# Optimization experiments

Measured on AMD Instinct MI355X. Metric: run time of the kernel, lower is better.

Reference implementation:

```python
import jax, jax.numpy as jnp
import numpy as np

N = 8192
D = 1024
TIME_DECAY = 86400.0
EPS = 1e-10


def setup_inputs() -> dict:
    key = jax.random.key(0)
    ks = jax.random.split(key, 8)
    x = jax.random.normal(ks[0], (N, D), dtype=jnp.float32)
    # timestamps spanning ~10 days so decay bias is non-trivial
    timestamps = jax.random.uniform(ks[1], (N,), dtype=jnp.float32) * (10.0 * TIME_DECAY)
    s = 1.0 / np.sqrt(D)
    Wq = jax.random.normal(ks[2], (D, D), dtype=jnp.float32) * s
    bq = jnp.zeros((D,), dtype=jnp.float32)
    Wk = jax.random.normal(ks[3], (D, D), dtype=jnp.float32) * s
    bk = jnp.zeros((D,), dtype=jnp.float32)
    Wv = jax.random.normal(ks[4], (D, D), dtype=jnp.float32) * s
    bv = jnp.zeros((D,), dtype=jnp.float32)
    return {"x": x, "timestamps": timestamps, "Wq": Wq, "bq": bq,
            "Wk": Wk, "bk": bk, "Wv": Wv, "bv": bv}


def reference(x, timestamps, Wq, bq, Wk, bk, Wv, bv):
    scale = jnp.asarray(D ** 0.5, x.dtype)
    # torch nn.Linear: y = x @ W.T + b
    Q = x @ Wq.T + bq          # [N, D]
    K = x @ Wk.T + bk          # [N, D]
    V = x @ Wv.T + bv          # [N, D]
    time_diff = timestamps[:, None] - timestamps[None, :]   # [N, N]
    time_decay = jnp.exp(-jnp.abs(time_diff) / TIME_DECAY)  # [N, N]
    scores = (Q @ K.T) / scale + jnp.log(time_decay + EPS)  # [N, N]
    attn = jax.nn.softmax(scores, axis=-1)
    return attn @ V
```

## Files before the change

### kernel.cpp

```cpp
#include <hip/hip_runtime.h>


using half8   = __attribute__((ext_vector_type(8))) _Float16;
using half4   = __attribute__((ext_vector_type(4))) _Float16;
using floatx4 = __attribute__((ext_vector_type(4))) float;

__device__ __forceinline__ void gload_lds16(const void* g, void* l) {
  __builtin_amdgcn_global_load_lds((const __attribute__((address_space(1))) void*)g,
                                   (__attribute__((address_space(3))) void*)l,
                                   16, 0, 0);
}

template<int N> __device__ __forceinline__ void waitv() {
  if constexpr (N == 8)      asm volatile("s_waitcnt vmcnt(8)" ::: "memory");
  else if constexpr (N == 6) asm volatile("s_waitcnt vmcnt(6)" ::: "memory");
  else                       asm volatile("s_waitcnt vmcnt(0)" ::: "memory");
}

#define MFMA16(ar, br, accrow)                                              \
  _Pragma("unroll")                                                         \
  for (int i_ = 0; i_ < 4; ++i_)                                            \
    _Pragma("unroll")                                                       \
    for (int j_ = 0; j_ < 4; ++j_)                                          \
      accrow[i_][j_] = __builtin_amdgcn_mfma_f32_16x16x32_f16(              \
          ar[i_], br[j_], accrow[i_][j_], 0, 0, 0);

__device__ __forceinline__ void kloop_s(
    const _Float16* __restrict__ A, const _Float16* __restrict__ B,
    long rowBase, long colBase, int lda, int ldb, int K,
    _Float16* __restrict__ As, _Float16* __restrict__ Bs,
    floatx4 (&acc)[8][4])
{
  const int tid = threadIdx.x;
  const int w = tid >> 6, lane = tid & 63;
  const int q = lane >> 4, l15 = lane & 15;
  const int wr = w >> 2, wcn = w & 3;

  const int sc = ((lane & 7) ^ (lane >> 3)) << 3;
  const _Float16* Agp[4]; const _Float16* Bgp[4];
#pragma unroll
  for (int p = 0; p < 4; ++p) {
    Agp[p] = A + (rowBase + p * 64 + (tid >> 3)) * (long)lda + sc;
    Bgp[p] = B + (colBase + p * 64 + (tid >> 3)) * (long)ldb + sc;
  }
  const int ldsOff = tid * 8;

  const int aRow = wr * 128 + l15;
  const int bRow = wcn * 64 + l15;
  const int cx = l15 & 7;
  const int pc0 = (q ^ cx) << 3, pc1 = ((4 + q) ^ cx) << 3;

  auto stageA = [&](int t) {
    _Float16* dst = As + (t & 1) * 16384;
    const int ko = t << 6;
#pragma unroll
    for (int p = 0; p < 4; ++p) gload_lds16(Agp[p] + ko, dst + p * 4096 + ldsOff);
  };
  auto stageB = [&](int t) {
    _Float16* dst = Bs + (t & 1) * 16384;
    const int ko = t << 6;
#pragma unroll
    for (int p = 0; p < 4; ++p) gload_lds16(Bgp[p] + ko, dst + p * 4096 + ldsOff);
  };

  const int NT = K >> 6;
  stageA(0); stageB(0); stageA(1); stageB(1);
  waitv<8>(); __builtin_amdgcn_s_barrier();

  for (int t = 0; t < NT; ++t) {
    const _Float16* Asl = As + (t & 1) * 16384;
    const _Float16* Bsl = Bs + (t & 1) * 16384;
    half8 b0[4], b1[4], a0lo[4], a0hi[4], a1lo[4], a1hi[4];

#pragma unroll
    for (int j = 0; j < 4; ++j) b0[j]   = *(const half8*)&Bsl[(bRow + 16 * j) * 64 + pc0];
#pragma unroll
    for (int i = 0; i < 4; ++i) a0lo[i] = *(const half8*)&Asl[(aRow + 16 * i) * 64 + pc0];
#pragma unroll
    for (int i = 0; i < 4; ++i) a0hi[i] = *(const half8*)&Asl[(aRow + 16 * (4 + i)) * 64 + pc0];
    {
      floatx4 (&alo)[4][4] = *(floatx4(*)[4][4])&acc[0];
      MFMA16(a0lo, b0, alo);
    }
#pragma unroll
    for (int j = 0; j < 4; ++j) b1[j]   = *(const half8*)&Bsl[(bRow + 16 * j) * 64 + pc1];
#pragma unroll
    for (int i = 0; i < 4; ++i) a1lo[i] = *(const half8*)&Asl[(aRow + 16 * i) * 64 + pc1];
    {
      floatx4 (&ahi)[4][4] = *(floatx4(*)[4][4])&acc[4];
      MFMA16(a0hi, b0, ahi);
    }
#pragma unroll
    for (int i = 0; i < 4; ++i) a1hi[i] = *(const half8*)&Asl[(aRow + 16 * (4 + i)) * 64 + pc1];
    {
      floatx4 (&alo)[4][4] = *(floatx4(*)[4][4])&acc[0];
      MFMA16(a1lo, b1, alo);
    }

    asm volatile("s_waitcnt lgkmcnt(0)" ::: "memory");
    __builtin_amdgcn_s_barrier();
    if (t + 2 < NT) { stageA(t + 2); stageB(t + 2); }
    {
      floatx4 (&ahi)[4][4] = *(floatx4(*)[4][4])&acc[4];
      MFMA16(a1hi, b1, ahi);
    }
    if (t < NT - 1) {
      if (t + 2 < NT) waitv<8>(); else waitv<0>();
      __builtin_amdgcn_s_barrier();
    }
  }
}

__device__ __forceinline__ void kloop_v(
    const _Float16* __restrict__ A, const _Float16* __restrict__ B,
    long rowBase, long colBase, int lda, int ldb, int K,
    _Float16* __restrict__ As, _Float16* __restrict__ Bs,
    floatx4 (&acc)[4][4])
{
  const int tid = threadIdx.x;
  const int w = tid >> 6, lane = tid & 63;
  const int q = lane >> 4, l15 = lane & 15;
  const int wr = w >> 1, wcn = w & 1;

  const int sc = ((lane & 7) ^ (lane >> 3)) << 3;
  const _Float16* Agp[4]; const _Float16* Bgp[2];
#pragma unroll
  for (int p = 0; p < 4; ++p)
    Agp[p] = A + (rowBase + p * 64 + (tid >> 3)) * (long)lda + sc;
#pragma unroll
  for (int p = 0; p < 2; ++p)
    Bgp[p] = B + (colBase + p * 64 + (tid >> 3)) * (long)ldb + sc;
  const int ldsOff = tid * 8;

  const int aRow = wr * 64 + l15;
  const int bRow = wcn * 64 + l15;
  const int cx = l15 & 7;
  const int pc0 = (q ^ cx) << 3, pc1 = ((4 + q) ^ cx) << 3;

  auto stage = [&](int t) {
    const int s = t % 3;
    _Float16* dA = As + s * 16384;
    _Float16* dB = Bs + s * 8192;
    const int ko = t << 6;
#pragma unroll
    for (int p = 0; p < 4; ++p) gload_lds16(Agp[p] + ko, dA + p * 4096 + ldsOff);
#pragma unroll
    for (int p = 0; p < 2; ++p) gload_lds16(Bgp[p] + ko, dB + p * 4096 + ldsOff);
  };

  const int NT = K >> 6;
  stage(0); stage(1);
  waitv<6>(); __builtin_amdgcn_s_barrier();

  for (int t = 0; t < NT; ++t) {
    const int s = t % 3;
    const _Float16* Asl = As + s * 16384;
    const _Float16* Bsl = Bs + s * 8192;
    half8 b0[4], b1[4], a0[4], a1[4];
#pragma unroll
    for (int j = 0; j < 4; ++j) b0[j] = *(const half8*)&Bsl[(bRow + 16 * j) * 64 + pc0];
#pragma unroll
    for (int i = 0; i < 4; ++i) a0[i] = *(const half8*)&Asl[(aRow + 16 * i) * 64 + pc0];
#pragma unroll
    for (int j = 0; j < 4; ++j) b1[j] = *(const half8*)&Bsl[(bRow + 16 * j) * 64 + pc1];
#pragma unroll
    for (int i = 0; i < 4; ++i) a1[i] = *(const half8*)&Asl[(aRow + 16 * i) * 64 + pc1];
    MFMA16(a0, b0, acc);
    if (t + 2 < NT) stage(t + 2);
    MFMA16(a1, b1, acc);
    if (t < NT - 1) {
      if (t + 2 < NT) waitv<6>(); else waitv<0>();
      __builtin_amdgcn_s_barrier();
    }
  }
}

template<int BIAS_MODE, int OUT_MODE>
__global__ __launch_bounds__(512, 2)
void gemmS_k(const _Float16* __restrict__ A, const _Float16* __restrict__ B,
             void* __restrict__ Cout, const float* __restrict__ bias,
             int lda, int ldb, int ldc, int K, float outScale)
{
  __shared__ __align__(16) _Float16 As[2 * 16384];
  __shared__ __align__(16) _Float16 Bs[2 * 16384];
  const long rowBase = (long)blockIdx.y * 256;
  const long colBase = (long)blockIdx.x * 256;

  floatx4 acc[8][4] = {};
  kloop_s(A, B, rowBase, colBase, lda, ldb, K, As, Bs, acc);

  const int tid = threadIdx.x;
  const int w = tid >> 6, lane = tid & 63;
  const int q = lane >> 4, l15 = lane & 15;
  const int wr = w >> 2, wcn = w & 3;
#pragma unroll
  for (int i = 0; i < 8; ++i) {
#pragma unroll
    for (int r = 0; r < 4; ++r) {
      const long rowg = rowBase + wr * 128 + 16 * i + q * 4 + r;
#pragma unroll
      for (int j = 0; j < 4; ++j) {
        const long colg = colBase + wcn * 64 + 16 * j + l15;
        float v = acc[i][j][r];
        if (BIAS_MODE == 1) v += bias[colg];
        if (BIAS_MODE == 2) v += bias[rowg];
        v *= outScale;
        if (OUT_MODE == 2) ((float*)Cout)[rowg * ldc + colg] = v;
        else               ((_Float16*)Cout)[rowg * ldc + colg] = (_Float16)v;
      }
    }
  }
}

template<int BIAS_MODE, int OUT_MODE, int SWZ>
__global__ __launch_bounds__(512, 2)
void gemmV_k(const _Float16* __restrict__ A, const _Float16* __restrict__ B,
             void* __restrict__ Cout, const float* __restrict__ bias,
             int lda, int ldb, int ldc, int K, float outScale)
{
  __shared__ __align__(16) _Float16 As[3 * 16384];
  __shared__ __align__(16) _Float16 Bs[3 * 8192];

  int tx, ty;
  if (SWZ) {
    const int bflat = blockIdx.y * gridDim.x + blockIdx.x;
    ty = bflat % gridDim.y;
    tx = bflat / gridDim.y;
  } else {
    tx = blockIdx.x; ty = blockIdx.y;
  }
  const long rowBase = (long)ty * 256;
  const long colBase = (long)tx * 128;

  floatx4 acc[4][4] = {};
  kloop_v(A, B, rowBase, colBase, lda, ldb, K, As, Bs, acc);

  const int tid = threadIdx.x;
  const int w = tid >> 6, lane = tid & 63;
  const int q = lane >> 4, l15 = lane & 15;
  const int wr = w >> 1, wcn = w & 1;
#pragma unroll
  for (int i = 0; i < 4; ++i) {
#pragma unroll
    for (int r = 0; r < 4; ++r) {
      const long rowg = rowBase + wr * 64 + 16 * i + q * 4 + r;
#pragma unroll
      for (int j = 0; j < 4; ++j) {
        const long colg = colBase + wcn * 64 + 16 * j + l15;
        float v = acc[i][j][r];
        if (BIAS_MODE == 1) v += bias[colg];
        if (BIAS_MODE == 2) v += bias[rowg];
        if (BIAS_MODE == 3) v *= bias[rowg];
        v *= outScale;
        if (OUT_MODE == 2) ((float*)Cout)[rowg * ldc + colg] = v;
        else               ((_Float16*)Cout)[rowg * ldc + colg] = (_Float16)v;
      }
    }
  }
}

__global__ __launch_bounds__(512, 2)
void gemm_statsS_k(const _Float16* __restrict__ A, const _Float16* __restrict__ B,
                   const float* __restrict__ ts, _Float16* __restrict__ U,
                   float* __restrict__ part, int lda, int ldb, int N, int K,
                   float qkScale)
{
  __shared__ __align__(16) _Float16 As[2 * 16384];
  __shared__ __align__(16) _Float16 Bs[2 * 16384];
  const int tid = threadIdx.x;
  const long rowBase = (long)blockIdx.y * 256;
  const long colBase = (long)blockIdx.x * 256;

  floatx4 acc[8][4] = {};
  kloop_s(A, B, rowBase, colBase, lda, ldb, K, As, Bs, acc);

  const int w = tid >> 6, lane = tid & 63;
  const int q = lane >> 4, l15 = lane & 15;
  const int wr = w >> 2, wcn = w & 3;
  const float inv_td = 1.0f / 86400.0f;

  float tc[4];
#pragma unroll
  for (int j = 0; j < 4; ++j) tc[j] = ts[colBase + wcn * 64 + 16 * j + l15];

  float* sl = (float*)As;
  __syncthreads();
#pragma unroll
  for (int i = 0; i < 8; ++i) {
#pragma unroll
    for (int r = 0; r < 4; ++r) {
      const int rowl = wr * 128 + 16 * i + q * 4 + r;
      const float tr = ts[rowBase + rowl];
      float ls = 0.0f;
#pragma unroll
      for (int j = 0; j < 4; ++j) {
        const int coll = wcn * 64 + 16 * j + l15;
        const float sv = acc[i][j][r] * qkScale
                       - fabsf(tr - tc[j]) * inv_td - 4.0f;
        const float u = __expf(sv);
        ls += u;
        U[(rowBase + rowl) * (long)N + (colBase + coll)] = (_Float16)u;
      }
      for (int mask = 1; mask <= 8; mask <<= 1)
        ls += __shfl_xor(ls, mask, 64);
      if (l15 == 0) sl[(wr * 4 + wcn) * 128 + 16 * i + 4 * q + r] = ls;
    }
  }
  __syncthreads();
  if (tid < 256) {
    const int band = tid & 127, hi = tid >> 7;
    part[(rowBase + tid) * 32 + blockIdx.x] =
        sl[(hi * 4 + 0) * 128 + band] + sl[(hi * 4 + 1) * 128 + band] +
        sl[(hi * 4 + 2) * 128 + band] + sl[(hi * 4 + 3) * 128 + band];
  }
}

__global__ void combine_k(const float* __restrict__ part, float* __restrict__ invL) {
  const int r = blockIdx.x * 256 + threadIdx.x;
  float L = 0.0f;
  for (int c = 0; c < 32; ++c) L += part[(long)r * 32 + c];
  invL[r] = 1.0f / L;
}

__global__ void cvt_k(const float* __restrict__ in, _Float16* __restrict__ out, int n) {
  const int i = (blockIdx.x * 256 + threadIdx.x) * 4;
  if (i >= n) return;
  const float4 v = *(const float4*)(in + i);
  half4 o = { (_Float16)v.x, (_Float16)v.y, (_Float16)v.z, (_Float16)v.w };
  *(half4*)(out + i) = o;
}

extern "C" void kernel_launch(void* const* d_in, const int* in_sizes, int n_in,
                              void* d_out, int out_size, void* d_ws, size_t ws_size,
                              hipStream_t stream)
{
  (void)in_sizes; (void)n_in; (void)out_size; (void)ws_size;
  const int N = 8192, D = 1024;
  const float* x  = (const float*)d_in[0];
  const float* ts = (const float*)d_in[1];
  const float* Wq = (const float*)d_in[2];
  const float* bq = (const float*)d_in[3];
  const float* Wk = (const float*)d_in[4];
  const float* bk = (const float*)d_in[5];
  const float* Wv = (const float*)d_in[6];
  const float* bv = (const float*)d_in[7];

  char* p = (char*)d_ws;
  auto grab = [&](size_t bytes) {
    char* r = p;
    p += (bytes + 255) & ~(size_t)255;
    return r;
  };
  _Float16* xh    = (_Float16*)grab((size_t)N * D * 2);
  _Float16* wqkh  = (_Float16*)grab((size_t)2 * D * D * 2);
  _Float16* wvh   = (_Float16*)grab((size_t)D * D * 2);
  _Float16* QKcat = (_Float16*)grab((size_t)N * 2 * D * 2);
  _Float16* VTh   = (_Float16*)grab((size_t)D * N * 2);
  _Float16* Uh    = (_Float16*)grab((size_t)N * N * 2);
  float*    part  = (float*)grab((size_t)N * 32 * sizeof(float));
  float*    invL  = (float*)grab((size_t)N * sizeof(float));
  float*    bcat  = (float*)grab((size_t)2 * D * sizeof(float));

  cvt_k<<<N * D / 1024, 256, 0, stream>>>(x,  xh,  N * D);
  cvt_k<<<D * D / 1024, 256, 0, stream>>>(Wq, wqkh,         D * D);
  cvt_k<<<D * D / 1024, 256, 0, stream>>>(Wk, wqkh + D * D, D * D);
  cvt_k<<<D * D / 1024, 256, 0, stream>>>(Wv, wvh, D * D);
  hipMemcpyAsync(bcat,     bq, D * sizeof(float), hipMemcpyDeviceToDevice, stream);
  hipMemcpyAsync(bcat + D, bk, D * sizeof(float), hipMemcpyDeviceToDevice, stream);

  dim3 blk(512);
  gemmS_k<1, 0><<<dim3(2 * D / 256, N / 256), blk, 0, stream>>>(
      xh, wqkh, QKcat, bcat, D, D, 2 * D, D, 1.0f);
  gemmV_k<2, 0, 0><<<dim3(N / 128, D / 256), blk, 0, stream>>>(
      wvh, xh, VTh, bv, D, D, N, D, 1.0f);
  gemm_statsS_k<<<dim3(N / 256, N / 256), blk, 0, stream>>>(
      QKcat, QKcat + D, ts, Uh, part, 2 * D, 2 * D, N, D, 1.0f / 32.0f);
  combine_k<<<N / 256, 256, 0, stream>>>(part, invL);
  gemmV_k<3, 2, 1><<<dim3(D / 128, N / 256), blk, 0, stream>>>(
      Uh, VTh, d_out, invL, N, N, D, N, 1.0f);
}
```

Before: 464.3 us.

## Switch GEMM inner loops from 16x16x32 to 32x32x16 MFMA tiles

Replaces the 16x16x32 f16 MFMA instructions with 32x32x16 ones across the score, value and projection GEMMs. Per-wave LDS fragment loads, swizzle offsets, accumulator layout and every epilogue (including the exp/stats epilogue and its row reduction) are rewritten for the 32x32 output layout. The larger MFMA shape cuts LDS reads per FLOP and the instruction count. In exchange it changes register pressure and how loads interleave with MFMAs.

```diff
diff --git a/kernel.cpp b/kernel.cpp
--- a/kernel.cpp
+++ b/kernel.cpp
@@ -1,9 +1,9 @@
 #include <hip/hip_runtime.h>
 
 
-using half8   = __attribute__((ext_vector_type(8))) _Float16;
-using half4   = __attribute__((ext_vector_type(4))) _Float16;
-using floatx4 = __attribute__((ext_vector_type(4))) float;
+using half8    = __attribute__((ext_vector_type(8))) _Float16;
+using half4    = __attribute__((ext_vector_type(4))) _Float16;
+using floatx16 = __attribute__((ext_vector_type(16))) float;
 
 __device__ __forceinline__ void gload_lds16(const void* g, void* l) {
   __builtin_amdgcn_global_load_lds((const __attribute__((address_space(1))) void*)g,
@@ -17,23 +17,15 @@
   else                       asm volatile("s_waitcnt vmcnt(0)" ::: "memory");
 }
 
-#define MFMA16(ar, br, accrow)                                              \
-  _Pragma("unroll")                                                         \
-  for (int i_ = 0; i_ < 4; ++i_)                                            \
-    _Pragma("unroll")                                                       \
-    for (int j_ = 0; j_ < 4; ++j_)                                          \
-      accrow[i_][j_] = __builtin_amdgcn_mfma_f32_16x16x32_f16(              \
-          ar[i_], br[j_], accrow[i_][j_], 0, 0, 0);
-
 __device__ __forceinline__ void kloop_s(
     const _Float16* __restrict__ A, const _Float16* __restrict__ B,
     long rowBase, long colBase, int lda, int ldb, int K,
     _Float16* __restrict__ As, _Float16* __restrict__ Bs,
-    floatx4 (&acc)[8][4])
-{
-  const int tid = threadIdx.x;
-  const int w = tid >> 6, lane = tid & 63;
-  const int q = lane >> 4, l15 = lane & 15;
+    floatx16 (&acc)[4][2])
+{
+  const int tid = threadIdx.x;
+  const int w = tid >> 6, lane = tid & 63;
+  const int l31 = lane & 31, hi = lane >> 5, l7 = lane & 7;
   const int wr = w >> 2, wcn = w & 3;
 
   const int sc = ((lane & 7) ^ (lane >> 3)) << 3;
@@ -45,10 +37,11 @@
   }
   const int ldsOff = tid * 8;
 
-  const int aRow = wr * 128 + l15;
-  const int bRow = wcn * 64 + l15;
-  const int cx = l15 & 7;
-  const int pc0 = (q ^ cx) << 3, pc1 = ((4 + q) ^ cx) << 3;
+  const int aRow = wr * 128 + l31;
+  const int bRow = wcn * 64 + l31;
+  int pcs[4];
+#pragma unroll
+  for (int ks = 0; ks < 4; ++ks) pcs[ks] = (((ks << 1) | hi) ^ l7) << 3;
 
   auto stageA = [&](int t) {
     _Float16* dst = As + (t & 1) * 16384;
@@ -70,44 +63,39 @@
   for (int t = 0; t < NT; ++t) {
     const _Float16* Asl = As + (t & 1) * 16384;
     const _Float16* Bsl = Bs + (t & 1) * 16384;
-    half8 b0[4], b1[4], a0lo[4], a0hi[4], a1lo[4], a1hi[4];
-
-#pragma unroll
-    for (int j = 0; j < 4; ++j) b0[j]   = *(const half8*)&Bsl[(bRow + 16 * j) * 64 + pc0];
-#pragma unroll
-    for (int i = 0; i < 4; ++i) a0lo[i] = *(const half8*)&Asl[(aRow + 16 * i) * 64 + pc0];
-#pragma unroll
-    for (int i = 0; i < 4; ++i) a0hi[i] = *(const half8*)&Asl[(aRow + 16 * (4 + i)) * 64 + pc0];
-    {
-      floatx4 (&alo)[4][4] = *(floatx4(*)[4][4])&acc[0];
-      MFMA16(a0lo, b0, alo);
-    }
-#pragma unroll
-    for (int j = 0; j < 4; ++j) b1[j]   = *(const half8*)&Bsl[(bRow + 16 * j) * 64 + pc1];
-#pragma unroll
-    for (int i = 0; i < 4; ++i) a1lo[i] = *(const half8*)&Asl[(aRow + 16 * i) * 64 + pc1];
-    {
-      floatx4 (&ahi)[4][4] = *(floatx4(*)[4][4])&acc[4];
-      MFMA16(a0hi, b0, ahi);
-    }
-#pragma unroll
-    for (int i = 0; i < 4; ++i) a1hi[i] = *(const half8*)&Asl[(aRow + 16 * (4 + i)) * 64 + pc1];
-    {
-      floatx4 (&alo)[4][4] = *(floatx4(*)[4][4])&acc[0];
-      MFMA16(a1lo, b1, alo);
-    }
-
+    half8 a[4][4], b[2][4];
+
+#define RD_G(ks)                                                             \
+    _Pragma("unroll")                                                        \
+    for (int j = 0; j < 2; ++j)                                              \
+      b[j][ks] = *(const half8*)&Bsl[(bRow + 32 * j) * 64 + pcs[ks]];        \
+    _Pragma("unroll")                                                        \
+    for (int i = 0; i < 4; ++i)                                              \
+      a[i][ks] = *(const half8*)&Asl[(aRow + 32 * i) * 64 + pcs[ks]];
+#define MM_G(ks)                                                             \
+    _Pragma("unroll")                                                        \
+    for (int i = 0; i < 4; ++i)                                              \
+      _Pragma("unroll")                                                      \
+      for (int j = 0; j < 2; ++j)                                            \
+        acc[i][j] = __builtin_amdgcn_mfma_f32_32x32x16_f16(                  \
+            a[i][ks], b[j][ks], acc[i][j], 0, 0, 0);
+
+    RD_G(0) RD_G(1)
+    MM_G(0)
+    RD_G(2)
+    MM_G(1)
+    RD_G(3)
+    MM_G(2)
     asm volatile("s_waitcnt lgkmcnt(0)" ::: "memory");
     __builtin_amdgcn_s_barrier();
     if (t + 2 < NT) { stageA(t + 2); stageB(t + 2); }
-    {
-      floatx4 (&ahi)[4][4] = *(floatx4(*)[4][4])&acc[4];
-      MFMA16(a1hi, b1, ahi);
-    }
+    MM_G(3)
     if (t < NT - 1) {
       if (t + 2 < NT) waitv<8>(); else waitv<0>();
       __builtin_amdgcn_s_barrier();
     }
+#undef RD_G
+#undef MM_G
   }
 }
 
@@ -115,11 +103,11 @@
     const _Float16* __restrict__ A, const _Float16* __restrict__ B,
     long rowBase, long colBase, int lda, int ldb, int K,
     _Float16* __restrict__ As, _Float16* __restrict__ Bs,
-    floatx4 (&acc)[4][4])
-{
-  const int tid = threadIdx.x;
-  const int w = tid >> 6, lane = tid & 63;
-  const int q = lane >> 4, l15 = lane & 15;
+    floatx16 (&acc)[2][2])
+{
+  const int tid = threadIdx.x;
+  const int w = tid >> 6, lane = tid & 63;
+  const int l31 = lane & 31, hi = lane >> 5, l7 = lane & 7;
   const int wr = w >> 1, wcn = w & 1;
 
   const int sc = ((lane & 7) ^ (lane >> 3)) << 3;
@@ -132,10 +120,11 @@
     Bgp[p] = B + (colBase + p * 64 + (tid >> 3)) * (long)ldb + sc;
   const int ldsOff = tid * 8;
 
-  const int aRow = wr * 64 + l15;
-  const int bRow = wcn * 64 + l15;
-  const int cx = l15 & 7;
-  const int pc0 = (q ^ cx) << 3, pc1 = ((4 + q) ^ cx) << 3;
+  const int aRow = wr * 64 + l31;
+  const int bRow = wcn * 64 + l31;
+  int pcs[4];
+#pragma unroll
+  for (int ks = 0; ks < 4; ++ks) pcs[ks] = (((ks << 1) | hi) ^ l7) << 3;
 
   auto stage = [&](int t) {
     const int s = t % 3;
@@ -156,18 +145,31 @@
     const int s = t % 3;
     const _Float16* Asl = As + s * 16384;
     const _Float16* Bsl = Bs + s * 8192;
-    half8 b0[4], b1[4], a0[4], a1[4];
-#pragma unroll
-    for (int j = 0; j < 4; ++j) b0[j] = *(const half8*)&Bsl[(bRow + 16 * j) * 64 + pc0];
-#pragma unroll
-    for (int i = 0; i < 4; ++i) a0[i] = *(const half8*)&Asl[(aRow + 16 * i) * 64 + pc0];
-#pragma unroll
-    for (int j = 0; j < 4; ++j) b1[j] = *(const half8*)&Bsl[(bRow + 16 * j) * 64 + pc1];
-#pragma unroll
-    for (int i = 0; i < 4; ++i) a1[i] = *(const half8*)&Asl[(aRow + 16 * i) * 64 + pc1];
-    MFMA16(a0, b0, acc);
+    half8 a[2][4], b[2][4];
+#pragma unroll
+    for (int ks = 0; ks < 4; ++ks) {
+#pragma unroll
+      for (int j = 0; j < 2; ++j)
+        b[j][ks] = *(const half8*)&Bsl[(bRow + 32 * j) * 64 + pcs[ks]];
+#pragma unroll
+      for (int i = 0; i < 2; ++i)
+        a[i][ks] = *(const half8*)&Asl[(aRow + 32 * i) * 64 + pcs[ks]];
+    }
+#pragma unroll
+    for (int ks = 0; ks < 2; ++ks)
+#pragma unroll
+      for (int i = 0; i < 2; ++i)
+#pragma unroll
+        for (int j = 0; j < 2; ++j)
+          acc[i][j] = __builtin_amdgcn_mfma_f32_32x32x16_f16(a[i][ks], b[j][ks], acc[i][j], 0, 0, 0);
     if (t + 2 < NT) stage(t + 2);
-    MFMA16(a1, b1, acc);
+#pragma unroll
+    for (int ks = 2; ks < 4; ++ks)
+#pragma unroll
+      for (int i = 0; i < 2; ++i)
+#pragma unroll
+        for (int j = 0; j < 2; ++j)
+          acc[i][j] = __builtin_amdgcn_mfma_f32_32x32x16_f16(a[i][ks], b[j][ks], acc[i][j], 0, 0, 0);
     if (t < NT - 1) {
       if (t + 2 < NT) waitv<6>(); else waitv<0>();
       __builtin_amdgcn_s_barrier();
@@ -186,22 +188,22 @@
   const long rowBase = (long)blockIdx.y * 256;
   const long colBase = (long)blockIdx.x * 256;
 
-  floatx4 acc[8][4] = {};
+  floatx16 acc[4][2] = {};
   kloop_s(A, B, rowBase, colBase, lda, ldb, K, As, Bs, acc);
 
   const int tid = threadIdx.x;
   const int w = tid >> 6, lane = tid & 63;
-  const int q = lane >> 4, l15 = lane & 15;
+  const int l31 = lane & 31, hi = lane >> 5;
   const int wr = w >> 2, wcn = w & 3;
 #pragma unroll
-  for (int i = 0; i < 8; ++i) {
-#pragma unroll
-    for (int r = 0; r < 4; ++r) {
-      const long rowg = rowBase + wr * 128 + 16 * i + q * 4 + r;
-#pragma unroll
-      for (int j = 0; j < 4; ++j) {
-        const long colg = colBase + wcn * 64 + 16 * j + l15;
-        float v = acc[i][j][r];
+  for (int i = 0; i < 4; ++i) {
+#pragma unroll
+    for (int reg = 0; reg < 16; ++reg) {
+      const long rowg = rowBase + wr * 128 + 32 * i + (reg & 3) + 8 * (reg >> 2) + 4 * hi;
+#pragma unroll
+      for (int j = 0; j < 2; ++j) {
+        const long colg = colBase + wcn * 64 + 32 * j + l31;
+        float v = acc[i][j][reg];
         if (BIAS_MODE == 1) v += bias[colg];
         if (BIAS_MODE == 2) v += bias[rowg];
         v *= outScale;
@@ -232,22 +234,22 @@
   const long rowBase = (long)ty * 256;
   const long colBase = (long)tx * 128;
 
-  floatx4 acc[4][4] = {};
+  floatx16 acc[2][2] = {};
   kloop_v(A, B, rowBase, colBase, lda, ldb, K, As, Bs, acc);
 
   const int tid = threadIdx.x;
   const int w = tid >> 6, lane = tid & 63;
-  const int q = lane >> 4, l15 = lane & 15;
+  const int l31 = lane & 31, hi = lane >> 5;
   const int wr = w >> 1, wcn = w & 1;
 #pragma unroll
-  for (int i = 0; i < 4; ++i) {
-#pragma unroll
-    for (int r = 0; r < 4; ++r) {
-      const long rowg = rowBase + wr * 64 + 16 * i + q * 4 + r;
-#pragma unroll
-      for (int j = 0; j < 4; ++j) {
-        const long colg = colBase + wcn * 64 + 16 * j + l15;
-        float v = acc[i][j][r];
+  for (int i = 0; i < 2; ++i) {
+#pragma unroll
+    for (int reg = 0; reg < 16; ++reg) {
+      const long rowg = rowBase + wr * 64 + 32 * i + (reg & 3) + 8 * (reg >> 2) + 4 * hi;
+#pragma unroll
+      for (int j = 0; j < 2; ++j) {
+        const long colg = colBase + wcn * 64 + 32 * j + l31;
+        float v = acc[i][j][reg];
         if (BIAS_MODE == 1) v += bias[colg];
         if (BIAS_MODE == 2) v += bias[rowg];
         if (BIAS_MODE == 3) v *= bias[rowg];
@@ -271,47 +273,47 @@
   const long rowBase = (long)blockIdx.y * 256;
   const long colBase = (long)blockIdx.x * 256;
 
-  floatx4 acc[8][4] = {};
+  floatx16 acc[4][2] = {};
   kloop_s(A, B, rowBase, colBase, lda, ldb, K, As, Bs, acc);
 
   const int w = tid >> 6, lane = tid & 63;
-  const int q = lane >> 4, l15 = lane & 15;
+  const int l31 = lane & 31, hi = lane >> 5;
   const int wr = w >> 2, wcn = w & 3;
   const float inv_td = 1.0f / 86400.0f;
 
-  float tc[4];
-#pragma unroll
-  for (int j = 0; j < 4; ++j) tc[j] = ts[colBase + wcn * 64 + 16 * j + l15];
+  float tc[2];
+#pragma unroll
+  for (int j = 0; j < 2; ++j) tc[j] = ts[colBase + wcn * 64 + 32 * j + l31];
 
   float* sl = (float*)As;
   __syncthreads();
 #pragma unroll
-  for (int i = 0; i < 8; ++i) {
-#pragma unroll
-    for (int r = 0; r < 4; ++r) {
-      const int rowl = wr * 128 + 16 * i + q * 4 + r;
+  for (int i = 0; i < 4; ++i) {
+#pragma unroll
+    for (int reg = 0; reg < 16; ++reg) {
+      const int rowl = wr * 128 + 32 * i + (reg & 3) + 8 * (reg >> 2) + 4 * hi;
       const float tr = ts[rowBase + rowl];
       float ls = 0.0f;
 #pragma unroll
-      for (int j = 0; j < 4; ++j) {
-        const int coll = wcn * 64 + 16 * j + l15;
-        const float sv = acc[i][j][r] * qkScale
+      for (int j = 0; j < 2; ++j) {
+        const int coll = wcn * 64 + 32 * j + l31;
+        const float sv = acc[i][j][reg] * qkScale
                        - fabsf(tr - tc[j]) * inv_td - 4.0f;
         const float u = __expf(sv);
         ls += u;
         U[(rowBase + rowl) * (long)N + (colBase + coll)] = (_Float16)u;
       }
-      for (int mask = 1; mask <= 8; mask <<= 1)
+      for (int mask = 1; mask <= 16; mask <<= 1)
         ls += __shfl_xor(ls, mask, 64);
-      if (l15 == 0) sl[(wr * 4 + wcn) * 128 + 16 * i + 4 * q + r] = ls;
+      if (l31 == 0) sl[(wr * 4 + wcn) * 128 + 32 * i + (reg & 3) + 8 * (reg >> 2) + 4 * hi] = ls;
     }
   }
   __syncthreads();
   if (tid < 256) {
-    const int band = tid & 127, hi = tid >> 7;
+    const int band = tid & 127, hib = tid >> 7;
     part[(rowBase + tid) * 32 + blockIdx.x] =
-        sl[(hi * 4 + 0) * 128 + band] + sl[(hi * 4 + 1) * 128 + band] +
-        sl[(hi * 4 + 2) * 128 + band] + sl[(hi * 4 + 3) * 128 + band];
+        sl[(hib * 4 + 0) * 128 + band] + sl[(hib * 4 + 1) * 128 + band] +
+        sl[(hib * 4 + 2) * 128 + band] + sl[(hib * 4 + 3) * 128 + band];
   }
 }
 
```

Measured after the change: 526.0 us. 13.3% more time.
